# Kernel tuning notes

Hardware: AMD Instinct MI355X
Metric: run time of the kernel (lower is better)

The kernel has to match this reference:

```python
import jax, jax.numpy as jnp
import numpy as np

B, IN, CTRL, M, V, OUT = 2048, 64, 512, 1024, 64, 64


def setup_inputs() -> dict:
    key = jax.random.key(0)
    ks = jax.random.split(key, 20)
    s = 0.05  # small param scale for numerical stability

    def rn(k, shape, scale):
        return jax.random.normal(k, shape, dtype=jnp.float32) * scale

    return {
        # forward args
        "x": rn(ks[0], (B, IN), 1.0),
        "h_prev": rn(ks[1], (B, CTRL), 0.1),
        "c_prev": rn(ks[2], (B, CTRL), 0.1),
        "read_weights_prev": jax.nn.softmax(rn(ks[3], (B, M), 1.0), axis=1),
        # parameters
        "memory": rn(ks[4], (M, V), 1.0),
        "W_ih": rn(ks[5], (4 * CTRL, IN + V), s),
        "b_ih": rn(ks[6], (4 * CTRL,), s),
        "W_hh": rn(ks[7], (4 * CTRL, CTRL), s),
        "b_hh": rn(ks[8], (4 * CTRL,), s),
        "W_read": rn(ks[9], (M, CTRL), s),
        "b_read": rn(ks[10], (M,), s),
        "W_write": rn(ks[11], (M, CTRL), s),
        "b_write": rn(ks[12], (M,), s),
        "W_erase": rn(ks[13], (V, CTRL), s),
        "b_erase": rn(ks[14], (V,), s),
        "W_add": rn(ks[15], (V, CTRL), s),
        "b_add": rn(ks[16], (V,), s),
        "W_out": rn(ks[17], (OUT, CTRL + V), s),
        "b_out": rn(ks[18], (OUT,), s),
    }


def reference(x, h_prev, c_prev, read_weights_prev, memory,
              W_ih, b_ih, W_hh, b_hh,
              W_read, b_read, W_write, b_write,
              W_erase, b_erase, W_add, b_add,
              W_out, b_out):
    # read with previous weights on pre-write memory: [B,M] @ [M,V] -> [B,V]
    read_prev = read_weights_prev @ memory
    inp = jnp.concatenate([x, read_prev], axis=1)  # [B, IN+V]

    # LSTMCell (PyTorch gate order: i, f, g, o)
    gates = inp @ W_ih.T + b_ih + h_prev @ W_hh.T + b_hh  # [B, 4*CTRL]
    i, f, g, o = jnp.split(gates, 4, axis=1)
    i = jax.nn.sigmoid(i)
    f = jax.nn.sigmoid(f)
    g = jnp.tanh(g)
    o = jax.nn.sigmoid(o)
    c = f * c_prev + i * g
    h = o * jnp.tanh(c)

    # addressing + erase/add vectors
    read_w = jax.nn.softmax(h @ W_read.T + b_read, axis=1)    # [B,M]
    write_w = jax.nn.softmax(h @ W_write.T + b_write, axis=1)  # [B,M]
    erase = jax.nn.sigmoid(h @ W_erase.T + b_erase)            # [B,V]
    add = jnp.tanh(h @ W_add.T + b_add)                        # [B,V]

    # outer-product erase/add memory update: [B,M,V]
    w = write_w[:, :, None]
    mem_new = memory[None, :, :] * (1.0 - w * erase[:, None, :]) + w * add[:, None, :]

    # read with new weights on post-write memory
    read_new = jnp.einsum('bm,bmv->bv', read_w, mem_new)

    out = jnp.concatenate([h, read_new], axis=1) @ W_out.T + b_out  # [B,OUT]
    return out
```

## Files before the change

### kernel.cpp

```cpp
#include <hip/hip_runtime.h>
#include <hip/hip_bf16.h>


typedef unsigned short u16;
typedef __attribute__((ext_vector_type(8))) short bf16x8;
typedef __attribute__((ext_vector_type(4))) float f32x4;

#define MFMA_BF16(a, b, c) __builtin_amdgcn_mfma_f32_16x16x32_bf16((a), (b), (c), 0, 0, 0)
#define LDW 136
#define SLDW 520

__device__ __forceinline__ void dma16(const void* g, void* l) {
    __builtin_amdgcn_global_load_lds(
        (const __attribute__((address_space(1))) unsigned int*)g,
        (__attribute__((address_space(3))) unsigned int*)l, 16, 0, 0);
}

__device__ __forceinline__ u16 f2bf(float f) {
    union { float f; unsigned int u; } a; a.f = f;
    return (u16)((a.u + 0x7FFFu + ((a.u >> 16) & 1u)) >> 16);
}

__device__ __forceinline__ void pack_store4(float a0, float a1, float a2, float a3, u16* d) {
    union { __hip_bfloat162 h[2]; uint2 u; } cv;
    cv.h[0] = __float22bfloat162_rn(make_float2(a0, a1));
    cv.h[1] = __float22bfloat162_rn(make_float2(a2, a3));
    *(uint2*)d = cv.u;
}

__device__ __forceinline__ void cvt4(const float* __restrict__ s, u16* __restrict__ d) {
    float4 v = *(const float4*)s;
    pack_store4(v.x, v.y, v.z, v.w, d);
}

__device__ __forceinline__ uint4 cvt8u(const float* __restrict__ s) {
    float4 v0 = *(const float4*)(s);
    float4 v1 = *(const float4*)(s + 4);
    union { __hip_bfloat162 h[4]; uint4 u; } r;
    r.h[0] = __float22bfloat162_rn(make_float2(v0.x, v0.y));
    r.h[1] = __float22bfloat162_rn(make_float2(v0.z, v0.w));
    r.h[2] = __float22bfloat162_rn(make_float2(v1.x, v1.y));
    r.h[3] = __float22bfloat162_rn(make_float2(v1.z, v1.w));
    return r.u;
}

__device__ __forceinline__ uint4 cvt8u_sum4(const float* __restrict__ p, int off) {
    float4 a0 = *(const float4*)(p + off);
    float4 a1 = *(const float4*)(p + 131072 + off);
    float4 a2 = *(const float4*)(p + 262144 + off);
    float4 a3 = *(const float4*)(p + 393216 + off);
    float4 b0 = *(const float4*)(p + off + 4);
    float4 b1 = *(const float4*)(p + 131072 + off + 4);
    float4 b2 = *(const float4*)(p + 262144 + off + 4);
    float4 b3 = *(const float4*)(p + 393216 + off + 4);
    float4 s0{a0.x + a1.x + a2.x + a3.x, a0.y + a1.y + a2.y + a3.y,
              a0.z + a1.z + a2.z + a3.z, a0.w + a1.w + a2.w + a3.w};
    float4 s1{b0.x + b1.x + b2.x + b3.x, b0.y + b1.y + b2.y + b3.y,
              b0.z + b1.z + b2.z + b3.z, b0.w + b1.w + b2.w + b3.w};
    union { __hip_bfloat162 h[4]; uint4 u; } r;
    r.h[0] = __float22bfloat162_rn(make_float2(s0.x, s0.y));
    r.h[1] = __float22bfloat162_rn(make_float2(s0.z, s0.w));
    r.h[2] = __float22bfloat162_rn(make_float2(s1.x, s1.y));
    r.h[3] = __float22bfloat162_rn(make_float2(s1.z, s1.w));
    return r.u;
}

__device__ __forceinline__ void bfu4_to_f8(uint4 u, float* f) {
    f[0] = __uint_as_float(u.x << 16); f[1] = __uint_as_float(u.x & 0xffff0000u);
    f[2] = __uint_as_float(u.y << 16); f[3] = __uint_as_float(u.y & 0xffff0000u);
    f[4] = __uint_as_float(u.z << 16); f[5] = __uint_as_float(u.z & 0xffff0000u);
    f[6] = __uint_as_float(u.w << 16); f[7] = __uint_as_float(u.w & 0xffff0000u);
}

__device__ __forceinline__ uint4 pack8(const float* v) {
    union { __hip_bfloat162 h[4]; uint4 u; } r;
#pragma unroll
    for (int j = 0; j < 4; ++j) r.h[j] = __float22bfloat162_rn(make_float2(v[2 * j], v[2 * j + 1]));
    return r.u;
}

__device__ __forceinline__ float sigf(float x) { return 1.f / (1.f + __expf(-x)); }
__device__ __forceinline__ float fast_tanh(float x) { return 1.f - 2.f / (__expf(2.f * x) + 1.f); }

#define PIPE_BAR_PRE_CNT()  do {                                              \
    asm volatile("s_waitcnt vmcnt(6) lgkmcnt(0)" ::: "memory");               \
    __builtin_amdgcn_s_barrier();                                             \
    __builtin_amdgcn_sched_barrier(0);                                        \
} while (0)
#define PIPE_BAR_PRE_ZERO() do {                                              \
    asm volatile("s_waitcnt vmcnt(0) lgkmcnt(0)" ::: "memory");               \
    __builtin_amdgcn_s_barrier();                                             \
    __builtin_amdgcn_sched_barrier(0);                                        \
} while (0)
#define PIPE_BAR_POST() do {                                                  \
    __builtin_amdgcn_sched_barrier(0);                                        \
    asm volatile("s_waitcnt lgkmcnt(0)" ::: "memory");                        \
    __builtin_amdgcn_s_barrier();                                             \
    __builtin_amdgcn_sched_barrier(0);                                        \
} while (0)

__device__ __forceinline__ void convert_unit(int t,
    const float* __restrict__ x, const float* __restrict__ h_prev,
    const float* __restrict__ W_ih, const float* __restrict__ W_hh,
    const float* __restrict__ W_read, const float* __restrict__ W_write,
    const float* __restrict__ W_erase, const float* __restrict__ W_add,
    const float* __restrict__ W_out, const float* __restrict__ memory,
    u16* x_t, u16* ht_t, u16* wcat_t, u16* Wcat2_t, u16* Wo_rn, u16* memt)
{
    if (t < 32768) {
        int r = t >> 4, c = (t & 15) * 4;
        cvt4(x + r * 64 + c, x_t + ((r >> 7) * 8 + (c >> 3)) * 1024 + (r & 127) * 8 + (c & 7));
        return;
    }
    t -= 32768;
    if (t < 262144) {
        int r = t >> 7, c = (t & 127) * 4;
        cvt4(h_prev + r * 512 + c, ht_t + ((r >> 7) * 64 + (c >> 3)) * 1024 + (r & 127) * 8 + (c & 7));
        return;
    }
    t -= 262144;
    if (t < 65536) {
        int r = t >> 5, c = (t & 31) * 4;
        int g = r >> 9, j = r & 511;
        int bn = j >> 4, row64 = (g << 4) + (j & 15);
        int cd = (c < 64) ? c + 64 : c - 64;
        cvt4(W_ih + r * 128 + c, wcat_t + (bn * 5) * 8192 + (cd >> 3) * 512 + row64 * 8 + (cd & 7));
        return;
    }
    t -= 65536;
    if (t < 262144) {
        int r = t >> 7, c = (t & 127) * 4;
        int g = r >> 9, j = r & 511;
        int bn = j >> 4, row64 = (g << 4) + (j & 15);
        int cd = 128 + c;
        cvt4(W_hh + r * 512 + c, wcat_t + (bn * 5 + (cd >> 7)) * 8192 + ((cd >> 3) & 15) * 512 + row64 * 8 + (cd & 7));
        return;
    }
    t -= 262144;
    if (t < 131072) {
        int r = t >> 7, c = (t & 127) * 4;
        cvt4(W_read + t * 4, Wcat2_t + ((r >> 6) * 4 + (c >> 7)) * 8192 + ((c >> 3) & 15) * 512 + (r & 63) * 8 + (c & 7));
        return;
    }
    t -= 131072;
    if (t < 131072) {
        int r = t >> 7, c = (t & 127) * 4;
        cvt4(W_write + t * 4, Wcat2_t + ((16 + (r >> 6)) * 4 + (c >> 7)) * 8192 + ((c >> 3) & 15) * 512 + (r & 63) * 8 + (c & 7));
        return;
    }
    t -= 131072;
    if (t < 8192) {
        int r = t >> 7, c = (t & 127) * 4;
        cvt4(W_erase + t * 4, Wcat2_t + (32 * 4 + (c >> 7)) * 8192 + ((c >> 3) & 15) * 512 + r * 8 + (c & 7));
        return;
    }
    t -= 8192;
    if (t < 8192) {
        int r = t >> 7, c = (t & 127) * 4;
        cvt4(W_add + t * 4, Wcat2_t + (33 * 4 + (c >> 7)) * 8192 + ((c >> 3) & 15) * 512 + r * 8 + (c & 7));
        return;
    }
    t -= 8192;
    if (t < 9216) {
        int r = t / 144, c = (t % 144) * 4;
        if (c < 512)
            cvt4(W_out + r * 576 + c, Wcat2_t + (34 * 4 + (c >> 7)) * 8192 + ((c >> 3) & 15) * 512 + r * 8 + (c & 7));
        else
            cvt4(W_out + r * 576 + c, Wo_rn + r * 64 + (c - 512));
        return;
    }
    t -= 9216;
    {
        int v = t >> 8, m = (t & 255) * 4;
        pack_store4(memory[m * 64 + v], memory[(m + 1) * 64 + v],
                    memory[(m + 2) * 64 + v], memory[(m + 3) * 64 + v], memt + v * 1024 + m);
    }
}

__global__ __launch_bounds__(256) void k_pre(
    const float* __restrict__ x, const float* __restrict__ h_prev, const float* __restrict__ rwp,
    const float* __restrict__ memory, const float* __restrict__ W_ih, const float* __restrict__ W_hh,
    const float* __restrict__ W_read, const float* __restrict__ W_write, const float* __restrict__ W_erase,
    const float* __restrict__ W_add, const float* __restrict__ W_out,
    u16* x_t, u16* ht_t, u16* wcat_t, u16* Wcat2_t, u16* Wo_rn, u16* memt, float* rp)
{
    __shared__ u16 As[64 * LDW];
    __shared__ u16 Bs[64 * LDW];
    const int tid = threadIdx.x;

    if (blockIdx.x < 128) {
        const int mb = blockIdx.x & 31, ks = blockIdx.x >> 5;
        const int w = tid >> 6, lane = tid & 63;
        const int lrow = lane & 15, lq = lane >> 4;
        const int m0 = mb * 64, k0 = ks * 256;
        const int m_loc = tid >> 1, v0 = (tid & 1) * 32;
        f32x4 acc[4] = {};
        for (int kt = 0; kt < 2; ++kt) {
#pragma unroll
            for (int i = 0; i < 4; ++i) {
                int idx = i * 256 + tid, r = idx >> 4, c = (idx & 15) * 8;
                *(uint4*)(&As[r * LDW + c]) = cvt8u(rwp + (m0 + r) * 1024 + k0 + kt * 128 + c);
            }
#pragma unroll
            for (int j = 0; j < 8; ++j) {
                float4 q = *(const float4*)(memory + (k0 + kt * 128 + m_loc) * 64 + v0 + 4 * j);
                Bs[(v0 + 4 * j + 0) * LDW + m_loc] = f2bf(q.x);
                Bs[(v0 + 4 * j + 1) * LDW + m_loc] = f2bf(q.y);
                Bs[(v0 + 4 * j + 2) * LDW + m_loc] = f2bf(q.z);
                Bs[(v0 + 4 * j + 3) * LDW + m_loc] = f2bf(q.w);
            }
            __syncthreads();
#pragma unroll
            for (int kk = 0; kk < 128; kk += 32) {
                bf16x8 a  = *(const bf16x8*)(&As[(16 * w + lrow) * LDW + kk + 8 * lq]);
                bf16x8 b0 = *(const bf16x8*)(&Bs[(lrow) * LDW + kk + 8 * lq]);
                bf16x8 b1 = *(const bf16x8*)(&Bs[(16 + lrow) * LDW + kk + 8 * lq]);
                bf16x8 b2 = *(const bf16x8*)(&Bs[(32 + lrow) * LDW + kk + 8 * lq]);
                bf16x8 b3 = *(const bf16x8*)(&Bs[(48 + lrow) * LDW + kk + 8 * lq]);
                acc[0] = MFMA_BF16(a, b0, acc[0]);
                acc[1] = MFMA_BF16(a, b1, acc[1]);
                acc[2] = MFMA_BF16(a, b2, acc[2]);
                acc[3] = MFMA_BF16(a, b3, acc[3]);
            }
            __syncthreads();
        }
        float* rps = rp + ks * 131072;
#pragma unroll
        for (int nj = 0; nj < 4; ++nj)
#pragma unroll
            for (int r = 0; r < 4; ++r) {
                int row = m0 + 16 * w + 4 * lq + r, col = 16 * nj + lrow;
                rps[row * 64 + col] = acc[nj][r];
            }
        return;
    }

    for (int t = (blockIdx.x - 128) * 256 + tid; t < 926720; t += 512 * 256)
        convert_unit(t, x, h_prev, W_ih, W_hh, W_read, W_write, W_erase, W_add,
                     W_out, memory, x_t, ht_t, wcat_t, Wcat2_t, Wo_rn, memt);
}

__global__ __launch_bounds__(256) void k_gates(const u16* __restrict__ x_t, const u16* __restrict__ ht_t,
                                               const float* __restrict__ rp, const u16* __restrict__ wcat_t,
                                               const float* __restrict__ b_ih, const float* __restrict__ b_hh,
                                               const float* __restrict__ c_prev, u16* __restrict__ hrn_t)
{
    __shared__ u16 As[2][8192];
    __shared__ u16 Bs[2][4096];
    const int tid = threadIdx.x, w = tid >> 6, lane = tid & 63;
    const int lrow = lane & 15, lq = lane >> 4;
    const int mt = blockIdx.x, bn = blockIdx.y;
    const int m0 = mt * 128;
    f32x4 acc[2][4] = {};

#pragma unroll
    for (int i = 0; i < 4; ++i) {
        int cp = i * 256 + tid;
        *(uint4*)(&As[0][cp * 8]) = cvt8u_sum4(rp, (m0 + (cp & 127)) * 64 + (cp >> 7) * 8);
    }
#pragma unroll
    for (int i = 0; i < 2; ++i) {
        int cp = i * 256 + tid;
        dma16(wcat_t + (bn * 5) * 8192 + cp * 8, &Bs[0][(i * 256 + w * 64) * 8]);
    }

#pragma unroll
    for (int t = 0; t < 10; ++t) {
        if (t < 9) {
            const int tn = t + 1, b = tn & 1;
            const u16* asrc = (tn == 1) ? (x_t + mt * 8192)
                                        : (ht_t + mt * 65536 + (tn - 2) * 8192);
#pragma unroll
            for (int i = 0; i < 4; ++i) {
                int cp = i * 256 + tid;
                dma16(asrc + cp * 8, &As[b][(i * 256 + w * 64) * 8]);
            }
#pragma unroll
            for (int i = 0; i < 2; ++i) {
                int cp = i * 256 + tid;
                dma16(wcat_t + (bn * 5 + (tn >> 1)) * 8192 + (tn & 1) * 4096 + cp * 8,
                      &Bs[b][(i * 256 + w * 64) * 8]);
            }
            PIPE_BAR_PRE_CNT();
        } else {
            PIPE_BAR_PRE_ZERO();
        }
        const int b = t & 1;
#pragma unroll
        for (int kk = 0; kk < 64; kk += 32) {
            const int ob = (kk >> 3) + lq;
            bf16x8 a0 = *(const bf16x8*)(&As[b][ob * 1024 + (32 * w + lrow) * 8]);
            bf16x8 a1 = *(const bf16x8*)(&As[b][ob * 1024 + (32 * w + 16 + lrow) * 8]);
            bf16x8 b0 = *(const bf16x8*)(&Bs[b][ob * 512 + (lrow) * 8]);
            bf16x8 b1 = *(const bf16x8*)(&Bs[b][ob * 512 + (16 + lrow) * 8]);
            bf16x8 b2 = *(const bf16x8*)(&Bs[b][ob * 512 + (32 + lrow) * 8]);
            bf16x8 b3 = *(const bf16x8*)(&Bs[b][ob * 512 + (48 + lrow) * 8]);
            acc[0][0] = MFMA_BF16(a0, b0, acc[0][0]);
            acc[0][1] = MFMA_BF16(a0, b1, acc[0][1]);
            acc[0][2] = MFMA_BF16(a0, b2, acc[0][2]);
            acc[0][3] = MFMA_BF16(a0, b3, acc[0][3]);
            acc[1][0] = MFMA_BF16(a1, b0, acc[1][0]);
            acc[1][1] = MFMA_BF16(a1, b1, acc[1][1]);
            acc[1][2] = MFMA_BF16(a1, b2, acc[1][2]);
            acc[1][3] = MFMA_BF16(a1, b3, acc[1][3]);
        }
        PIPE_BAR_POST();
    }

    const int j = bn * 16 + lrow;
    const float bI = b_ih[j] + b_hh[j];
    const float bF = b_ih[512 + j] + b_hh[512 + j];
    const float bG = b_ih[1024 + j] + b_hh[1024 + j];
    const float bO = b_ih[1536 + j] + b_hh[1536 + j];
#pragma unroll
    for (int mi = 0; mi < 2; ++mi)
#pragma unroll
        for (int r = 0; r < 4; ++r) {
            int row = m0 + 32 * w + 16 * mi + 4 * lq + r;
            float ig = sigf(acc[mi][0][r] + bI);
            float fg = sigf(acc[mi][1][r] + bF);
            float gg = fast_tanh(acc[mi][2][r] + bG);
            float og = sigf(acc[mi][3][r] + bO);
            float c = fg * c_prev[row * 512 + j] + ig * gg;
            hrn_t[(row >> 7) * 65536 + (j >> 3) * 1024 + (row & 127) * 8 + (j & 7)] =
                f2bf(og * fast_tanh(c));
        }
}

__global__ __launch_bounds__(256) void k_heads(const u16* __restrict__ hrn_t, const u16* __restrict__ Wcat2_t,
                                               const float* __restrict__ b_read, const float* __restrict__ b_write,
                                               const float* __restrict__ b_erase, const float* __restrict__ b_add,
                                               const float* __restrict__ b_out,
                                               u16* __restrict__ pre_r, u16* __restrict__ pre_w,
                                               float* __restrict__ erase, float* __restrict__ add,
                                               float* __restrict__ out)
{
    __shared__ u16 As[2][8192];
    __shared__ u16 Bs[2][4096];
    const int tid = threadIdx.x, w = tid >> 6, lane = tid & 63;
    const int lrow = lane & 15, lq = lane >> 4;
    const int mt = blockIdx.x, bn = blockIdx.y;
    const int m0 = mt * 128;
    f32x4 acc[2][4] = {};

#pragma unroll
    for (int i = 0; i < 4; ++i) {
        int cp = i * 256 + tid;
        dma16(hrn_t + mt * 65536 + cp * 8, &As[0][(i * 256 + w * 64) * 8]);
    }
#pragma unroll
    for (int i = 0; i < 2; ++i) {
        int cp = i * 256 + tid;
        dma16(Wcat2_t + (bn * 4) * 8192 + cp * 8, &Bs[0][(i * 256 + w * 64) * 8]);
    }

#pragma unroll
    for (int t = 0; t < 8; ++t) {
        if (t < 7) {
            const int tn = t + 1, b = tn & 1;
#pragma unroll
            for (int i = 0; i < 4; ++i) {
                int cp = i * 256 + tid;
                dma16(hrn_t + mt * 65536 + tn * 8192 + cp * 8, &As[b][(i * 256 + w * 64) * 8]);
            }
#pragma unroll
            for (int i = 0; i < 2; ++i) {
                int cp = i * 256 + tid;
                dma16(Wcat2_t + (bn * 4 + (tn >> 1)) * 8192 + (tn & 1) * 4096 + cp * 8,
                      &Bs[b][(i * 256 + w * 64) * 8]);
            }
            PIPE_BAR_PRE_CNT();
        } else {
            PIPE_BAR_PRE_ZERO();
        }
        const int b = t & 1;
#pragma unroll
        for (int kk = 0; kk < 64; kk += 32) {
            const int ob = (kk >> 3) + lq;
            bf16x8 a0 = *(const bf16x8*)(&As[b][ob * 1024 + (32 * w + lrow) * 8]);
            bf16x8 a1 = *(const bf16x8*)(&As[b][ob * 1024 + (32 * w + 16 + lrow) * 8]);
            bf16x8 b0 = *(const bf16x8*)(&Bs[b][ob * 512 + (lrow) * 8]);
            bf16x8 b1 = *(const bf16x8*)(&Bs[b][ob * 512 + (16 + lrow) * 8]);
            bf16x8 b2 = *(const bf16x8*)(&Bs[b][ob * 512 + (32 + lrow) * 8]);
            bf16x8 b3 = *(const bf16x8*)(&Bs[b][ob * 512 + (48 + lrow) * 8]);
            acc[0][0] = MFMA_BF16(a0, b0, acc[0][0]);
            acc[0][1] = MFMA_BF16(a0, b1, acc[0][1]);
            acc[0][2] = MFMA_BF16(a0, b2, acc[0][2]);
            acc[0][3] = MFMA_BF16(a0, b3, acc[0][3]);
            acc[1][0] = MFMA_BF16(a1, b0, acc[1][0]);
            acc[1][1] = MFMA_BF16(a1, b1, acc[1][1]);
            acc[1][2] = MFMA_BF16(a1, b2, acc[1][2]);
            acc[1][3] = MFMA_BF16(a1, b3, acc[1][3]);
        }
        PIPE_BAR_POST();
    }

#pragma unroll
    for (int mi = 0; mi < 2; ++mi)
#pragma unroll
        for (int nj = 0; nj < 4; ++nj)
#pragma unroll
            for (int r = 0; r < 4; ++r) {
                int row = m0 + 32 * w + 16 * mi + 4 * lq + r;
                int col = bn * 64 + 16 * nj + lrow;
                float v = acc[mi][nj][r];
                if (bn < 16)       pre_r[row * 1024 + col] = f2bf(v + b_read[col]);
                else if (bn < 32)  pre_w[row * 1024 + (col - 1024)] = f2bf(v + b_write[col - 1024]);
                else if (bn == 32) erase[row * 64 + (col - 2048)] = sigf(v + b_erase[col - 2048]);
                else if (bn == 33) add[row * 64 + (col - 2112)] = fast_tanh(v + b_add[col - 2112]);
                else               out[row * 64 + (col - 2176)] = v + b_out[col - 2176];
            }
}

__global__ __launch_bounds__(256) void k_tail(const u16* __restrict__ pre_r, const u16* __restrict__ pre_w,
                                              const u16* __restrict__ memt, const u16* __restrict__ Wo_rn,
                                              const float* __restrict__ erase, const float* __restrict__ add,
                                              float* __restrict__ out)
{
    __shared__ u16 rwS[16 * SLDW];
    __shared__ u16 rw2S[16 * SLDW];
    __shared__ u16 BsP[64 * LDW];
    __shared__ u16 Ps[16 * 72];
    __shared__ float s_sh[16];
    const int tid = threadIdx.x, w = tid >> 6, lane = tid & 63;
    const int lrow = lane & 15, lq = lane >> 4;
    const int mb = blockIdx.x >> 1, kh = blockIdx.x & 1;
    const int m0 = mb * 16, k0 = kh * 512;

    {
        const int row = tid >> 4, c16 = tid & 15;
        const int row_g = m0 + row;
        const u16* prp = pre_r + row_g * 1024;
        const u16* pwp = pre_w + row_g * 1024;
        float vr[64], vw[64];
#pragma unroll
        for (int q = 0; q < 8; ++q) {
            bfu4_to_f8(*(const uint4*)(prp + q * 128 + c16 * 8), vr + 8 * q);
            bfu4_to_f8(*(const uint4*)(pwp + q * 128 + c16 * 8), vw + 8 * q);
        }
        float mr = vr[0], mw = vw[0];
#pragma unroll
        for (int i = 1; i < 64; ++i) { mr = fmaxf(mr, vr[i]); mw = fmaxf(mw, vw[i]); }
#pragma unroll
        for (int o = 1; o < 16; o <<= 1) {
            mr = fmaxf(mr, __shfl_xor(mr, o, 64));
            mw = fmaxf(mw, __shfl_xor(mw, o, 64));
        }
        float sr = 0.f, sw = 0.f;
#pragma unroll
        for (int i = 0; i < 64; ++i) {
            vr[i] = __expf(vr[i] - mr); sr += vr[i];
            vw[i] = __expf(vw[i] - mw); sw += vw[i];
        }
#pragma unroll
        for (int o = 1; o < 16; o <<= 1) {
            sr += __shfl_xor(sr, o, 64);
            sw += __shfl_xor(sw, o, 64);
        }
        const float isr = 1.f / sr, isw = 1.f / sw;
        float ss = 0.f;
#pragma unroll
        for (int q = 0; q < 8; ++q) {
            float a8[8], r8[8];
#pragma unroll
            for (int i = 0; i < 8; ++i) {
                float a = vr[8 * q + i] * isr;
                float r2 = a * (vw[8 * q + i] * isw);
                a8[i] = a; r8[i] = r2;
                ss += r2;
            }
            if ((q >> 2) == kh) {
                int cb = (q - 4 * kh) * 128 + c16 * 8;
                *(uint4*)(&rwS[row * SLDW + cb])  = pack8(a8);
                *(uint4*)(&rw2S[row * SLDW + cb]) = pack8(r8);
            }
        }
#pragma unroll
        for (int o = 1; o < 16; o <<= 1) ss += __shfl_xor(ss, o, 64);
        if (c16 == 0) s_sh[row] = ss;
    }
    __syncthreads();

    f32x4 acc1 = {}, acc2 = {};
    for (int kt = 0; kt < 4; ++kt) {
#pragma unroll
        for (int i = 0; i < 4; ++i) {
            int idx = i * 256 + tid, r = idx >> 4, c = (idx & 15) * 8;
            *(uint4*)(&BsP[r * LDW + c]) = *(const uint4*)(memt + r * 1024 + k0 + kt * 128 + c);
        }
        __syncthreads();
#pragma unroll
        for (int kk = 0; kk < 128; kk += 32) {
            bf16x8 a1 = *(const bf16x8*)(&rwS[lrow * SLDW + kt * 128 + kk + 8 * lq]);
            bf16x8 a2 = *(const bf16x8*)(&rw2S[lrow * SLDW + kt * 128 + kk + 8 * lq]);
            bf16x8 b  = *(const bf16x8*)(&BsP[(16 * w + lrow) * LDW + kk + 8 * lq]);
            acc1 = MFMA_BF16(a1, b, acc1);
            acc2 = MFMA_BF16(a2, b, acc2);
        }
        __syncthreads();
    }

#pragma unroll
    for (int r = 0; r < 4; ++r) {
        int row_l = 4 * lq + r, col = 16 * w + lrow;
        int row_g = m0 + row_l;
        float p = acc1[r] - erase[row_g * 64 + col] * acc2[r];
        if (kh == 0) p += add[row_g * 64 + col] * s_sh[row_l];
        Ps[row_l * 72 + col] = f2bf(p);
    }
#pragma unroll
    for (int i = 0; i < 2; ++i) {
        int idx = i * 256 + tid, r = idx >> 3, c = (idx & 7) * 8;
        *(uint4*)(&BsP[r * LDW + c]) = *(const uint4*)(Wo_rn + r * 64 + c);
    }
    __syncthreads();

    f32x4 acc3 = {};
#pragma unroll
    for (int kk = 0; kk < 64; kk += 32) {
        bf16x8 a = *(const bf16x8*)(&Ps[lrow * 72 + kk + 8 * lq]);
        bf16x8 b = *(const bf16x8*)(&BsP[(16 * w + lrow) * LDW + kk + 8 * lq]);
        acc3 = MFMA_BF16(a, b, acc3);
    }
#pragma unroll
    for (int r = 0; r < 4; ++r) {
        int row_g = m0 + 4 * lq + r, col = 16 * w + lrow;
        atomicAdd(&out[row_g * 64 + col], acc3[r]);
    }
}

extern "C" void kernel_launch(void* const* d_in, const int* in_sizes, int n_in,
                              void* d_out, int out_size, void* d_ws, size_t ws_size,
                              hipStream_t stream)
{
    const float* x        = (const float*)d_in[0];
    const float* h_prev   = (const float*)d_in[1];
    const float* c_prev   = (const float*)d_in[2];
    const float* rwp      = (const float*)d_in[3];
    const float* memory   = (const float*)d_in[4];
    const float* W_ih     = (const float*)d_in[5];
    const float* b_ih     = (const float*)d_in[6];
    const float* W_hh     = (const float*)d_in[7];
    const float* b_hh     = (const float*)d_in[8];
    const float* W_read   = (const float*)d_in[9];
    const float* b_read   = (const float*)d_in[10];
    const float* W_write  = (const float*)d_in[11];
    const float* b_write  = (const float*)d_in[12];
    const float* W_erase  = (const float*)d_in[13];
    const float* b_erase  = (const float*)d_in[14];
    const float* W_add    = (const float*)d_in[15];
    const float* b_add    = (const float*)d_in[16];
    const float* W_out    = (const float*)d_in[17];
    const float* b_out    = (const float*)d_in[18];
    float* out = (float*)d_out;

    char* wsp = (char*)d_ws;
    u16*   x_t     = (u16*)(wsp + 0);
    u16*   ht_t    = (u16*)(wsp + 262144);
    u16*   wcat_t  = (u16*)(wsp + 2359296);
    u16*   memt    = (u16*)(wsp + 4980736);
    u16*   Wcat2_t = (u16*)(wsp + 5111808);
    u16*   Wo_rn   = (u16*)(wsp + 7405568);
    float* rp      = (float*)(wsp + 7413760);
    u16*   hrn_t   = (u16*)(wsp + 9510912);
    u16*   pre_r   = (u16*)(wsp + 11608064);
    u16*   pre_w   = (u16*)(wsp + 15802368);
    float* erase   = (float*)(wsp + 19996672);
    float* add     = (float*)(wsp + 20520960);

    k_pre<<<640, 256, 0, stream>>>(x, h_prev, rwp, memory, W_ih, W_hh, W_read, W_write,
                                   W_erase, W_add, W_out,
                                   x_t, ht_t, wcat_t, Wcat2_t, Wo_rn, memt, rp);
    k_gates<<<dim3(16, 32), 256, 0, stream>>>(x_t, ht_t, rp, wcat_t, b_ih, b_hh, c_prev, hrn_t);
    k_heads<<<dim3(16, 35), 256, 0, stream>>>(hrn_t, Wcat2_t, b_read, b_write, b_erase, b_add, b_out,
                                              pre_r, pre_w, erase, add, out);
    k_tail<<<256, 256, 0, stream>>>(pre_r, pre_w, memt, Wo_rn, erase, add, out);
}
```

Measured before the change: 156.8 us.

## Drop split-K for read_prev GEMM and emit bf16 tiled layout for DMA

The read_prev GEMM in k_pre no longer splits K four ways into fp32 partials. Each of the 128 blocks now computes 16 full rows over all of K and writes bf16 directly in the tiled layout that k_gates consumes. k_gates can then load that A tile with async global-to-LDS DMA, instead of summing four fp32 partials and converting in registers. The cost is that each block now loops 8 times with only one MFMA per wave per k-step and reloads the whole memory matrix, so the k_pre GEMM part becomes longer and less efficient.

```diff
diff --git a/kernel.cpp b/kernel.cpp
--- a/kernel.cpp
+++ b/kernel.cpp
@@ -41,27 +41,6 @@
     r.h[1] = __float22bfloat162_rn(make_float2(v0.z, v0.w));
     r.h[2] = __float22bfloat162_rn(make_float2(v1.x, v1.y));
     r.h[3] = __float22bfloat162_rn(make_float2(v1.z, v1.w));
-    return r.u;
-}
-
-__device__ __forceinline__ uint4 cvt8u_sum4(const float* __restrict__ p, int off) {
-    float4 a0 = *(const float4*)(p + off);
-    float4 a1 = *(const float4*)(p + 131072 + off);
-    float4 a2 = *(const float4*)(p + 262144 + off);
-    float4 a3 = *(const float4*)(p + 393216 + off);
-    float4 b0 = *(const float4*)(p + off + 4);
-    float4 b1 = *(const float4*)(p + 131072 + off + 4);
-    float4 b2 = *(const float4*)(p + 262144 + off + 4);
-    float4 b3 = *(const float4*)(p + 393216 + off + 4);
-    float4 s0{a0.x + a1.x + a2.x + a3.x, a0.y + a1.y + a2.y + a3.y,
-              a0.z + a1.z + a2.z + a3.z, a0.w + a1.w + a2.w + a3.w};
-    float4 s1{b0.x + b1.x + b2.x + b3.x, b0.y + b1.y + b2.y + b3.y,
-              b0.z + b1.z + b2.z + b3.z, b0.w + b1.w + b2.w + b3.w};
-    union { __hip_bfloat162 h[4]; uint4 u; } r;
-    r.h[0] = __float22bfloat162_rn(make_float2(s0.x, s0.y));
-    r.h[1] = __float22bfloat162_rn(make_float2(s0.z, s0.w));
-    r.h[2] = __float22bfloat162_rn(make_float2(s1.x, s1.y));
-    r.h[3] = __float22bfloat162_rn(make_float2(s1.z, s1.w));
     return r.u;
 }
 
@@ -182,28 +161,27 @@
     const float* __restrict__ memory, const float* __restrict__ W_ih, const float* __restrict__ W_hh,
     const float* __restrict__ W_read, const float* __restrict__ W_write, const float* __restrict__ W_erase,
     const float* __restrict__ W_add, const float* __restrict__ W_out,
-    u16* x_t, u16* ht_t, u16* wcat_t, u16* Wcat2_t, u16* Wo_rn, u16* memt, float* rp)
+    u16* x_t, u16* ht_t, u16* wcat_t, u16* Wcat2_t, u16* Wo_rn, u16* memt, u16* rpt)
 {
     __shared__ u16 As[64 * LDW];
     __shared__ u16 Bs[64 * LDW];
     const int tid = threadIdx.x;
 
     if (blockIdx.x < 128) {
-        const int mb = blockIdx.x & 31, ks = blockIdx.x >> 5;
+        const int mb = blockIdx.x;
         const int w = tid >> 6, lane = tid & 63;
         const int lrow = lane & 15, lq = lane >> 4;
-        const int m0 = mb * 64, k0 = ks * 256;
+        const int m0 = mb * 16;
         const int m_loc = tid >> 1, v0 = (tid & 1) * 32;
-        f32x4 acc[4] = {};
-        for (int kt = 0; kt < 2; ++kt) {
-#pragma unroll
-            for (int i = 0; i < 4; ++i) {
-                int idx = i * 256 + tid, r = idx >> 4, c = (idx & 15) * 8;
-                *(uint4*)(&As[r * LDW + c]) = cvt8u(rwp + (m0 + r) * 1024 + k0 + kt * 128 + c);
+        f32x4 acc = {};
+        for (int kt = 0; kt < 8; ++kt) {
+            {
+                int r = tid >> 4, c = (tid & 15) * 8;
+                *(uint4*)(&As[r * LDW + c]) = cvt8u(rwp + (m0 + r) * 1024 + kt * 128 + c);
             }
 #pragma unroll
             for (int j = 0; j < 8; ++j) {
-                float4 q = *(const float4*)(memory + (k0 + kt * 128 + m_loc) * 64 + v0 + 4 * j);
+                float4 q = *(const float4*)(memory + (kt * 128 + m_loc) * 64 + v0 + 4 * j);
                 Bs[(v0 + 4 * j + 0) * LDW + m_loc] = f2bf(q.x);
                 Bs[(v0 + 4 * j + 1) * LDW + m_loc] = f2bf(q.y);
                 Bs[(v0 + 4 * j + 2) * LDW + m_loc] = f2bf(q.z);
@@ -212,26 +190,17 @@
             __syncthreads();
 #pragma unroll
             for (int kk = 0; kk < 128; kk += 32) {
-                bf16x8 a  = *(const bf16x8*)(&As[(16 * w + lrow) * LDW + kk + 8 * lq]);
-                bf16x8 b0 = *(const bf16x8*)(&Bs[(lrow) * LDW + kk + 8 * lq]);
-                bf16x8 b1 = *(const bf16x8*)(&Bs[(16 + lrow) * LDW + kk + 8 * lq]);
-                bf16x8 b2 = *(const bf16x8*)(&Bs[(32 + lrow) * LDW + kk + 8 * lq]);
-                bf16x8 b3 = *(const bf16x8*)(&Bs[(48 + lrow) * LDW + kk + 8 * lq]);
-                acc[0] = MFMA_BF16(a, b0, acc[0]);
-                acc[1] = MFMA_BF16(a, b1, acc[1]);
-                acc[2] = MFMA_BF16(a, b2, acc[2]);
-                acc[3] = MFMA_BF16(a, b3, acc[3]);
+                bf16x8 a = *(const bf16x8*)(&As[lrow * LDW + kk + 8 * lq]);
+                bf16x8 b = *(const bf16x8*)(&Bs[(16 * w + lrow) * LDW + kk + 8 * lq]);
+                acc = MFMA_BF16(a, b, acc);
             }
             __syncthreads();
         }
-        float* rps = rp + ks * 131072;
-#pragma unroll
-        for (int nj = 0; nj < 4; ++nj)
-#pragma unroll
-            for (int r = 0; r < 4; ++r) {
-                int row = m0 + 16 * w + 4 * lq + r, col = 16 * nj + lrow;
-                rps[row * 64 + col] = acc[nj][r];
-            }
+#pragma unroll
+        for (int r = 0; r < 4; ++r) {
+            int row = m0 + 4 * lq + r, v = 16 * w + lrow;
+            rpt[(row >> 7) * 8192 + (v >> 3) * 1024 + (row & 127) * 8 + (v & 7)] = f2bf(acc[r]);
+        }
         return;
     }
 
@@ -240,8 +209,8 @@
                      W_out, memory, x_t, ht_t, wcat_t, Wcat2_t, Wo_rn, memt);
 }
 
-__global__ __launch_bounds__(256) void k_gates(const u16* __restrict__ x_t, const u16* __restrict__ ht_t,
-                                               const float* __restrict__ rp, const u16* __restrict__ wcat_t,
+__global__ __launch_bounds__(256) void k_gates(const u16* __restrict__ rpt, const u16* __restrict__ x_t,
+                                               const u16* __restrict__ ht_t, const u16* __restrict__ wcat_t,
                                                const float* __restrict__ b_ih, const float* __restrict__ b_hh,
                                                const float* __restrict__ c_prev, u16* __restrict__ hrn_t)
 {
@@ -254,15 +223,11 @@
     f32x4 acc[2][4] = {};
 
 #pragma unroll
-    for (int i = 0; i < 4; ++i) {
-        int cp = i * 256 + tid;
-        *(uint4*)(&As[0][cp * 8]) = cvt8u_sum4(rp, (m0 + (cp & 127)) * 64 + (cp >> 7) * 8);
-    }
-#pragma unroll
-    for (int i = 0; i < 2; ++i) {
-        int cp = i * 256 + tid;
-        dma16(wcat_t + (bn * 5) * 8192 + cp * 8, &Bs[0][(i * 256 + w * 64) * 8]);
-    }
+    for (int i = 0; i < 4; ++i)
+        dma16(rpt + mt * 8192 + (i * 256 + tid) * 8, &As[0][(i * 256 + w * 64) * 8]);
+#pragma unroll
+    for (int i = 0; i < 2; ++i)
+        dma16(wcat_t + (bn * 5) * 8192 + (i * 256 + tid) * 8, &Bs[0][(i * 256 + w * 64) * 8]);
 
 #pragma unroll
     for (int t = 0; t < 10; ++t) {
@@ -271,16 +236,12 @@
             const u16* asrc = (tn == 1) ? (x_t + mt * 8192)
                                         : (ht_t + mt * 65536 + (tn - 2) * 8192);
 #pragma unroll
-            for (int i = 0; i < 4; ++i) {
-                int cp = i * 256 + tid;
-                dma16(asrc + cp * 8, &As[b][(i * 256 + w * 64) * 8]);
-            }
-#pragma unroll
-            for (int i = 0; i < 2; ++i) {
-                int cp = i * 256 + tid;
-                dma16(wcat_t + (bn * 5 + (tn >> 1)) * 8192 + (tn & 1) * 4096 + cp * 8,
+            for (int i = 0; i < 4; ++i)
+                dma16(asrc + (i * 256 + tid) * 8, &As[b][(i * 256 + w * 64) * 8]);
+#pragma unroll
+            for (int i = 0; i < 2; ++i)
+                dma16(wcat_t + (bn * 5 + (tn >> 1)) * 8192 + (tn & 1) * 4096 + (i * 256 + tid) * 8,
                       &Bs[b][(i * 256 + w * 64) * 8]);
-            }
             PIPE_BAR_PRE_CNT();
         } else {
             PIPE_BAR_PRE_ZERO();
@@ -344,31 +305,24 @@
     f32x4 acc[2][4] = {};
 
 #pragma unroll
-    for (int i = 0; i < 4; ++i) {
-        int cp = i * 256 + tid;
-        dma16(hrn_t + mt * 65536 + cp * 8, &As[0][(i * 256 + w * 64) * 8]);
-    }
-#pragma unroll
-    for (int i = 0; i < 2; ++i) {
-        int cp = i * 256 + tid;
-        dma16(Wcat2_t + (bn * 4) * 8192 + cp * 8, &Bs[0][(i * 256 + w * 64) * 8]);
-    }
+    for (int i = 0; i < 4; ++i)
+        dma16(hrn_t + mt * 65536 + (i * 256 + tid) * 8, &As[0][(i * 256 + w * 64) * 8]);
+#pragma unroll
+    for (int i = 0; i < 2; ++i)
+        dma16(Wcat2_t + (bn * 4) * 8192 + (i * 256 + tid) * 8, &Bs[0][(i * 256 + w * 64) * 8]);
 
 #pragma unroll
     for (int t = 0; t < 8; ++t) {
         if (t < 7) {
             const int tn = t + 1, b = tn & 1;
 #pragma unroll
-            for (int i = 0; i < 4; ++i) {
-                int cp = i * 256 + tid;
-                dma16(hrn_t + mt * 65536 + tn * 8192 + cp * 8, &As[b][(i * 256 + w * 64) * 8]);
-            }
-#pragma unroll
-            for (int i = 0; i < 2; ++i) {
-                int cp = i * 256 + tid;
-                dma16(Wcat2_t + (bn * 4 + (tn >> 1)) * 8192 + (tn & 1) * 4096 + cp * 8,
+            for (int i = 0; i < 4; ++i)
+                dma16(hrn_t + mt * 65536 + tn * 8192 + (i * 256 + tid) * 8,
+                      &As[b][(i * 256 + w * 64) * 8]);
+#pragma unroll
+            for (int i = 0; i < 2; ++i)
+                dma16(Wcat2_t + (bn * 4 + (tn >> 1)) * 8192 + (tn & 1) * 4096 + (i * 256 + tid) * 8,
                       &Bs[b][(i * 256 + w * 64) * 8]);
-            }
             PIPE_BAR_PRE_CNT();
         } else {
             PIPE_BAR_PRE_ZERO();
@@ -561,7 +515,7 @@
     u16*   memt    = (u16*)(wsp + 4980736);
     u16*   Wcat2_t = (u16*)(wsp + 5111808);
     u16*   Wo_rn   = (u16*)(wsp + 7405568);
-    float* rp      = (float*)(wsp + 7413760);
+    u16*   rpt     = (u16*)(wsp + 7413760);
     u16*   hrn_t   = (u16*)(wsp + 9510912);
     u16*   pre_r   = (u16*)(wsp + 11608064);
     u16*   pre_w   = (u16*)(wsp + 15802368);
@@ -570,8 +524,8 @@
 
     k_pre<<<640, 256, 0, stream>>>(x, h_prev, rwp, memory, W_ih, W_hh, W_read, W_write,
                                    W_erase, W_add, W_out,
-                                   x_t, ht_t, wcat_t, Wcat2_t, Wo_rn, memt, rp);
-    k_gates<<<dim3(16, 32), 256, 0, stream>>>(x_t, ht_t, rp, wcat_t, b_ih, b_hh, c_prev, hrn_t);
+                                   x_t, ht_t, wcat_t, Wcat2_t, Wo_rn, memt, rpt);
+    k_gates<<<dim3(16, 32), 256, 0, stream>>>(rpt, x_t, ht_t, wcat_t, b_ih, b_hh, c_prev, hrn_t);
     k_heads<<<dim3(16, 35), 256, 0, stream>>>(hrn_t, Wcat2_t, b_read, b_write, b_erase, b_add, b_out,
                                               pre_r, pre_w, erase, add, out);
     k_tail<<<256, 256, 0, stream>>>(pre_r, pre_w, memt, Wo_rn, erase, add, out);
```

Result: no change. 154.1 us (-1.7%).
